# Optimization experiments

Measured on AMD Instinct MI355X. Metric: run time of the kernel, lower is better.

## Reference

```python
import jax, jax.numpy as jnp
import numpy as np

# dims: batch B, seq T, d_model C, expert_hidden H, n_experts E (top-1 routing)
B, T, C, H, E = 1, 256, 1024, 2048, 8
STD = 0.02


def setup_inputs() -> dict:
    key = jax.random.key(0)
    ks = jax.random.split(key, 8)
    f32 = jnp.float32
    return {
        "x": jax.random.normal(ks[0], (B, T, C), f32),
        "up": jax.random.normal(ks[1], (E, H, C), f32) * STD,
        "gate": jax.random.normal(ks[2], (E, H, C), f32) * STD,
        "down": jax.random.normal(ks[3], (E, C, H), f32) * STD,
        "router": jax.random.normal(ks[4], (E, C), f32) * STD,
        "w_up_s": jax.random.normal(ks[5], (H, C), f32) * STD,
        "w_gate_s": jax.random.normal(ks[6], (H, C), f32) * STD,
        "w_down_s": jax.random.normal(ks[7], (C, H), f32) * STD,
    }


def reference(x, up, gate, down, router, w_up_s, w_gate_s, w_down_s):
    b, t, c = x.shape
    x_ = x.reshape(b * t, c)                      # [BT, C]
    # top-1 router (gates are implicitly 1.0)
    logits = x_ @ router.T                        # [BT, E]
    idx = jnp.argmax(logits, axis=-1)             # [BT]
    onehot = jax.nn.one_hot(idx, router.shape[0], dtype=x.dtype)  # [BT, E]
    # dense all-expert SwiGLU, combined with one-hot (same math as per-token gather)
    u = jnp.einsum('bc,ehc->ebh', x_, up)         # [E, BT, H]
    g = jnp.einsum('bc,ehc->ebh', x_, gate)       # [E, BT, H]
    h = jax.nn.silu(g) * u                        # [E, BT, H]
    ye = jnp.einsum('ebh,ech->ebc', h, down)      # [E, BT, C]
    y = jnp.einsum('ebc,be->bc', ye, onehot)      # [BT, C]
    # shared expert residual
    ys = (jax.nn.silu(x_ @ w_gate_s.T) * (x_ @ w_up_s.T)) @ w_down_s.T
    return (y + ys).reshape(b, t, c)
```

## Files before the change

kernel.cpp:

```cpp
#include <hip/hip_runtime.h>
#include <hip/hip_bf16.h>

#define T_TOK 256
#define C_DIM 1024
#define H_DIM 2048
#define E_NUM 8

typedef __attribute__((ext_vector_type(4))) float f32x4;
typedef __attribute__((ext_vector_type(8))) short short8;

#define WS_CNT    0
#define WS_LIST   1024
#define WS_XBF    16384
#define WS_HBUF   (1u<<20)
#define WS_HSBUF  (2u<<20)
#define WS_YS     (3u<<20)

__device__ __forceinline__ ushort f2bf(float f) {
    __hip_bfloat16 h = __float2bfloat16(f);
    return *reinterpret_cast<ushort*>(&h);
}

__device__ __forceinline__ ushort4 f2bf4(float4 v) {
    ushort4 r; r.x = f2bf(v.x); r.y = f2bf(v.y); r.z = f2bf(v.z); r.w = f2bf(v.w);
    return r;
}

__device__ __forceinline__ void gload16(const void* g, void* l) {
    __builtin_amdgcn_global_load_lds((const __attribute__((address_space(1))) void*)g,
                                     (__attribute__((address_space(3))) void*)l, 16, 0, 0);
}

#define MFMA(a, b, c) __builtin_amdgcn_mfma_f32_16x16x32_bf16((a), (b), (c), 0, 0, 0)

#define VMWAIT(N) do { asm volatile("s_waitcnt vmcnt(" #N ")" ::: "memory"); \
                       __builtin_amdgcn_sched_barrier(0); } while (0)
#define LGKWAIT() do { asm volatile("s_waitcnt lgkmcnt(0)" ::: "memory"); \
                       __builtin_amdgcn_sched_barrier(0); } while (0)
#define BAR() do { __builtin_amdgcn_s_barrier(); \
                   __builtin_amdgcn_sched_barrier(0); } while (0)

__global__ __launch_bounds__(256) void router_kernel(
    const float* __restrict__ x, const float* __restrict__ router,
    int* __restrict__ cnt, int* __restrict__ list, ushort* __restrict__ xbf)
{
    const int t = blockIdx.x;
    const int tid = threadIdx.x;
    float4 xv = reinterpret_cast<const float4*>(x + (size_t)t * C_DIM)[tid];
    *reinterpret_cast<ushort4*>(xbf + (size_t)t * C_DIM + tid * 4) = f2bf4(xv);

    float p[E_NUM];
#pragma unroll
    for (int e = 0; e < E_NUM; e++) {
        float4 rv = reinterpret_cast<const float4*>(router + (size_t)e * C_DIM)[tid];
        p[e] = xv.x * rv.x + xv.y * rv.y + xv.z * rv.z + xv.w * rv.w;
    }
#pragma unroll
    for (int e = 0; e < E_NUM; e++) {
#pragma unroll
        for (int off = 32; off >= 1; off >>= 1)
            p[e] += __shfl_down(p[e], off, 64);
    }
    __shared__ float red[E_NUM][4];
    const int lane = tid & 63, wv = tid >> 6;
    if (lane == 0) {
#pragma unroll
        for (int e = 0; e < E_NUM; e++) red[e][wv] = p[e];
    }
    __syncthreads();
    if (tid == 0) {
        float best = -3.4e38f; int bi = 0;
#pragma unroll
        for (int e = 0; e < E_NUM; e++) {
            float v = red[e][0] + red[e][1] + red[e][2] + red[e][3];
            if (v > best) { best = v; bi = e; }
        }
        int pos = atomicAdd(&cnt[bi], 1);
        list[bi * T_TOK + pos] = t;
    }
}

__global__ __launch_bounds__(256, 2) void ug_mfma(
    const ushort* __restrict__ xbf, const float* __restrict__ up, const float* __restrict__ gate,
    const float* __restrict__ w_up_s, const float* __restrict__ w_gate_s,
    const int* __restrict__ cnt, const int* __restrict__ list,
    ushort* __restrict__ hbuf, ushort* __restrict__ hsbuf)
{
    const int e = blockIdx.x, by = blockIdx.y, tt = blockIdx.z;
    const bool sh = (e == E_NUM);
    const int n = sh ? T_TOK : cnt[e];
    if (tt * 32 >= n) return;
    const int tid = threadIdx.x, lane = tid & 63, wv = tid >> 6;
    const int lc = lane & 15, kg = lane >> 4;

    __shared__ __align__(16) char smem[65536];
    ushort* Xl  = (ushort*)smem;
    ushort* WuL = (ushort*)(smem + 32768);
    ushort* WgL = (ushort*)(smem + 49152);
    __shared__ int toks_s[32];

    if (tid < 32) {
        int t = tt * 32 + tid;
        toks_s[tid] = (t < n) ? (sh ? t : list[e * T_TOK + t]) : -1;
    }
    __syncthreads();

    const int h0 = by * 16;
    const float* __restrict__ ubase = (sh ? w_up_s   : up   + (size_t)e * H_DIM * C_DIM) + (size_t)h0 * C_DIM;
    const float* __restrict__ gbase = (sh ? w_gate_s : gate + (size_t)e * H_DIM * C_DIM) + (size_t)h0 * C_DIM;

    float4 wreg[8];
#define W_LOAD(tc) do { _Pragma("unroll") for (int i = 0; i < 8; i++) { \
        int row_ = wv * 4 + (i & 3); \
        const float* b_ = (i < 4) ? ubase : gbase; \
        wreg[i] = *reinterpret_cast<const float4*>(b_ + (size_t)row_ * C_DIM + (tc) * 256 + lane * 4); \
    } } while (0)

#define W_WRITE(bf) do { _Pragma("unroll") for (int i = 0; i < 8; i++) { \
        int row_ = wv * 4 + (i & 3); \
        ushort* WL_ = (i < 4) ? WuL : WgL; \
        int pos_ = ((lane >> 1) & ~7) | (((lane >> 1) ^ row_) & 7); \
        *reinterpret_cast<ushort4*>(WL_ + (bf) * 4096 + row_ * 256 + pos_ * 8 + (lane & 1) * 4) = f2bf4(wreg[i]); \
    } } while (0)

#define X_STAGE(tc, bf) do { _Pragma("unroll") for (int i = 0; i < 4; i++) { \
        int j_ = wv * 4 + i; \
        int row_ = 2 * j_ + (lane >> 5); \
        int p_ = lane & 31; \
        int su_ = (p_ & ~7) | ((p_ ^ row_) & 7); \
        int tok_ = toks_s[row_]; if (tok_ < 0) tok_ = 0; \
        gload16(xbf + (size_t)tok_ * C_DIM + (tc) * 256 + su_ * 8, (void*)(Xl + (bf) * 8192 + j_ * 512)); \
    } } while (0)

    f32x4 au0 = {0,0,0,0}, au1 = {0,0,0,0}, ag0 = {0,0,0,0}, ag1 = {0,0,0,0};
#define COMPUTE(bf) do { _Pragma("unroll") for (int k32 = 0; k32 < 2; k32++) { \
        int ku_ = wv * 8 + k32 * 4 + kg; \
        int up_ = (ku_ & ~7) | ((ku_ ^ lc) & 7); \
        short8 a0_ = *reinterpret_cast<const short8*>(Xl + (bf) * 8192 + lc * 256 + up_ * 8); \
        short8 a1_ = *reinterpret_cast<const short8*>(Xl + (bf) * 8192 + (16 + lc) * 256 + up_ * 8); \
        short8 bu_ = *reinterpret_cast<const short8*>(WuL + (bf) * 4096 + lc * 256 + up_ * 8); \
        short8 bg_ = *reinterpret_cast<const short8*>(WgL + (bf) * 4096 + lc * 256 + up_ * 8); \
        au0 = MFMA(a0_, bu_, au0); au1 = MFMA(a1_, bu_, au1); \
        ag0 = MFMA(a0_, bg_, ag0); ag1 = MFMA(a1_, bg_, ag1); \
    } } while (0)

    W_LOAD(0);
    X_STAGE(0, 0);
    VMWAIT(4);
    W_WRITE(0);
    W_LOAD(1);
    X_STAGE(1, 1);
    LGKWAIT();
    VMWAIT(12);
    BAR();

#pragma unroll
    for (int t = 0; t < 4; t++) {
        COMPUTE(t & 1);
        if (t < 3) {
            VMWAIT(4);
            W_WRITE((t + 1) & 1);
            if (t < 2) W_LOAD(t + 2);
            LGKWAIT();
        }
        BAR();
        if (t < 2) X_STAGE(t + 2, t & 1);
        if (t < 2)      { VMWAIT(12); }
        else if (t == 2){ VMWAIT(0);  }
        BAR();
    }

    f32x4* red = (f32x4*)smem;
    red[(wv * 4 + 0) * 64 + lane] = au0;
    red[(wv * 4 + 1) * 64 + lane] = au1;
    red[(wv * 4 + 2) * 64 + lane] = ag0;
    red[(wv * 4 + 3) * 64 + lane] = ag1;
    __syncthreads();
    if (tid < 128) {
        const int m = tid >> 6, ln = tid & 63, lc_ = ln & 15, kg_ = ln >> 4;
        f32x4 su = red[(0 + m) * 64 + ln];
        su += red[(4 + m) * 64 + ln];
        su += red[(8 + m) * 64 + ln];
        su += red[(12 + m) * 64 + ln];
        f32x4 sg = red[(2 + m) * 64 + ln];
        sg += red[(6 + m) * 64 + ln];
        sg += red[(10 + m) * 64 + ln];
        sg += red[(14 + m) * 64 + ln];
        ushort* __restrict__ outp = sh ? hsbuf : hbuf;
#pragma unroll
        for (int j = 0; j < 4; j++) {
            int tok = toks_s[m * 16 + kg_ * 4 + j];
            if (tok >= 0) {
                float g = sg[j], u = su[j];
                outp[(size_t)tok * H_DIM + h0 + lc_] = f2bf(u * (g / (1.f + __expf(-g))));
            }
        }
    }
#undef W_LOAD
#undef W_WRITE
#undef X_STAGE
#undef COMPUTE
}

__global__ __launch_bounds__(256, 2) void down_mfma(
    const float* __restrict__ dwn, const float* __restrict__ w_down_s,
    const ushort* __restrict__ hbuf, const ushort* __restrict__ hsbuf,
    const int* __restrict__ cnt, const int* __restrict__ list,
    float* __restrict__ y, float* __restrict__ yspart)
{
    const int e = blockIdx.x, by = blockIdx.y, tt = blockIdx.z;
    const bool sh = (e == E_NUM);
    const int n = sh ? T_TOK : cnt[e];
    if (tt * 32 >= n) return;
    const int tid = threadIdx.x, lane = tid & 63, wv = tid >> 6;
    const int lc = lane & 15, kg = lane >> 4;

    __shared__ __align__(16) char smem[49152];
    ushort* Hl  = (ushort*)smem;
    ushort* WdL = (ushort*)(smem + 32768);
    __shared__ int toks_s[32];

    if (tid < 32) {
        int t = tt * 32 + tid;
        toks_s[tid] = (t < n) ? (sh ? t : list[e * T_TOK + t]) : -1;
    }
    __syncthreads();

    const int c0 = by * 16;
    const float* __restrict__ dbase = (sh ? w_down_s : dwn + (size_t)e * C_DIM * H_DIM) + (size_t)c0 * H_DIM;
    const ushort* __restrict__ hin = sh ? hsbuf : hbuf;

    float4 wreg[4];
#define W_LOAD(tc) do { _Pragma("unroll") for (int i = 0; i < 4; i++) { \
        int row_ = wv * 4 + i; \
        wreg[i] = *reinterpret_cast<const float4*>(dbase + (size_t)row_ * H_DIM + (tc) * 256 + lane * 4); \
    } } while (0)

#define W_WRITE(bf) do { _Pragma("unroll") for (int i = 0; i < 4; i++) { \
        int row_ = wv * 4 + i; \
        int pos_ = ((lane >> 1) & ~7) | (((lane >> 1) ^ row_) & 7); \
        *reinterpret_cast<ushort4*>(WdL + (bf) * 4096 + row_ * 256 + pos_ * 8 + (lane & 1) * 4) = f2bf4(wreg[i]); \
    } } while (0)

#define H_STAGE(tc, bf) do { _Pragma("unroll") for (int i = 0; i < 4; i++) { \
        int j_ = wv * 4 + i; \
        int row_ = 2 * j_ + (lane >> 5); \
        int p_ = lane & 31; \
        int su_ = (p_ & ~7) | ((p_ ^ row_) & 7); \
        int tok_ = toks_s[row_]; if (tok_ < 0) tok_ = 0; \
        gload16(hin + (size_t)tok_ * H_DIM + (tc) * 256 + su_ * 8, (void*)(Hl + (bf) * 8192 + j_ * 512)); \
    } } while (0)

    f32x4 ac0 = {0,0,0,0}, ac1 = {0,0,0,0};
#define COMPUTE(bf) do { _Pragma("unroll") for (int k32 = 0; k32 < 2; k32++) { \
        int ku_ = wv * 8 + k32 * 4 + kg; \
        int up_ = (ku_ & ~7) | ((ku_ ^ lc) & 7); \
        short8 a0_ = *reinterpret_cast<const short8*>(Hl + (bf) * 8192 + lc * 256 + up_ * 8); \
        short8 a1_ = *reinterpret_cast<const short8*>(Hl + (bf) * 8192 + (16 + lc) * 256 + up_ * 8); \
        short8 bd_ = *reinterpret_cast<const short8*>(WdL + (bf) * 4096 + lc * 256 + up_ * 8); \
        ac0 = MFMA(a0_, bd_, ac0); ac1 = MFMA(a1_, bd_, ac1); \
    } } while (0)

    W_LOAD(0);
    H_STAGE(0, 0);
    VMWAIT(4);
    W_WRITE(0);
    W_LOAD(1);
    H_STAGE(1, 1);
    LGKWAIT();
    VMWAIT(8);
    BAR();

#pragma unroll
    for (int t = 0; t < 8; t++) {
        COMPUTE(t & 1);
        if (t < 7) {
            VMWAIT(4);
            W_WRITE((t + 1) & 1);
            if (t < 6) W_LOAD(t + 2);
            LGKWAIT();
        }
        BAR();
        if (t < 6) H_STAGE(t + 2, t & 1);
        if (t < 6)      { VMWAIT(8); }
        else if (t == 6){ VMWAIT(0); }
        BAR();
    }

    f32x4* red = (f32x4*)smem;
    red[(wv * 2 + 0) * 64 + lane] = ac0;
    red[(wv * 2 + 1) * 64 + lane] = ac1;
    __syncthreads();
    if (tid < 128) {
        const int m = tid >> 6, ln = tid & 63, lc_ = ln & 15, kg_ = ln >> 4;
        f32x4 s = red[(0 + m) * 64 + ln];
        s += red[(2 + m) * 64 + ln];
        s += red[(4 + m) * 64 + ln];
        s += red[(6 + m) * 64 + ln];
        float* __restrict__ outp = sh ? yspart : y;
#pragma unroll
        for (int j = 0; j < 4; j++) {
            int tok = toks_s[m * 16 + kg_ * 4 + j];
            if (tok >= 0) outp[(size_t)tok * C_DIM + c0 + lc_] = s[j];
        }
    }
#undef W_LOAD
#undef W_WRITE
#undef H_STAGE
#undef COMPUTE
}

__global__ __launch_bounds__(256) void add_kernel(float* __restrict__ y, const float* __restrict__ ys)
{
    int i = blockIdx.x * 256 + threadIdx.x;
    float4 a = reinterpret_cast<float4*>(y)[i];
    float4 b = reinterpret_cast<const float4*>(ys)[i];
    a.x += b.x; a.y += b.y; a.z += b.z; a.w += b.w;
    reinterpret_cast<float4*>(y)[i] = a;
}

extern "C" void kernel_launch(void* const* d_in, const int* in_sizes, int n_in,
                              void* d_out, int out_size, void* d_ws, size_t ws_size,
                              hipStream_t stream)
{
    const float* x        = (const float*)d_in[0];
    const float* up       = (const float*)d_in[1];
    const float* gate     = (const float*)d_in[2];
    const float* dwn      = (const float*)d_in[3];
    const float* router   = (const float*)d_in[4];
    const float* w_up_s   = (const float*)d_in[5];
    const float* w_gate_s = (const float*)d_in[6];
    const float* w_down_s = (const float*)d_in[7];

    char* ws = (char*)d_ws;
    int* cnt      = (int*)(ws + WS_CNT);
    int* list     = (int*)(ws + WS_LIST);
    ushort* xbf   = (ushort*)(ws + WS_XBF);
    ushort* hbuf  = (ushort*)(ws + WS_HBUF);
    ushort* hsbuf = (ushort*)(ws + WS_HSBUF);
    float* yspart = (float*)(ws + WS_YS);
    float* y = (float*)d_out;

    hipMemsetAsync(cnt, 0, E_NUM * sizeof(int), stream);
    router_kernel<<<T_TOK, 256, 0, stream>>>(x, router, cnt, list, xbf);
    ug_mfma<<<dim3(E_NUM + 1, H_DIM / 16, 8), 256, 0, stream>>>(
        xbf, up, gate, w_up_s, w_gate_s, cnt, list, hbuf, hsbuf);
    down_mfma<<<dim3(E_NUM + 1, C_DIM / 16, 8), 256, 0, stream>>>(
        dwn, w_down_s, hbuf, hsbuf, cnt, list, y, yspart);
    add_kernel<<<(T_TOK * C_DIM / 4) / 256, 256, 0, stream>>>(y, yspart);
}
```

Measured before the change: 92.57 us.

## Single-buffer ug_mfma LDS to raise occupancy and use nontemporal weight loads

Replaces the double-buffered LDS pipeline in the up/gate kernel with a single buffer, halving shared memory and raising launch bounds to three blocks per CU. The hand-scheduled waitcnt/barrier pipeline becomes a simple stage-write-sync-compute-sync loop that keeps only register prefetch of the next weight tile. Expert weights are now read with nontemporal loads to avoid cache pollution. This trades intra-block overlap of memory and MFMA for more resident waves, with added barrier stalls per iteration.

```diff
diff --git a/kernel.cpp b/kernel.cpp
--- a/kernel.cpp
+++ b/kernel.cpp
@@ -26,6 +26,11 @@
     return r;
 }
 
+__device__ __forceinline__ ushort4 f2bf4v(f32x4 v) {
+    ushort4 r; r.x = f2bf(v[0]); r.y = f2bf(v[1]); r.z = f2bf(v[2]); r.w = f2bf(v[3]);
+    return r;
+}
+
 __device__ __forceinline__ void gload16(const void* g, void* l) {
     __builtin_amdgcn_global_load_lds((const __attribute__((address_space(1))) void*)g,
                                      (__attribute__((address_space(3))) void*)l, 16, 0, 0);
@@ -80,7 +85,7 @@
     }
 }
 
-__global__ __launch_bounds__(256, 2) void ug_mfma(
+__global__ __launch_bounds__(256, 3) void ug_mfma(
     const ushort* __restrict__ xbf, const float* __restrict__ up, const float* __restrict__ gate,
     const float* __restrict__ w_up_s, const float* __restrict__ w_gate_s,
     const int* __restrict__ cnt, const int* __restrict__ list,
@@ -93,10 +98,10 @@
     const int tid = threadIdx.x, lane = tid & 63, wv = tid >> 6;
     const int lc = lane & 15, kg = lane >> 4;
 
-    __shared__ __align__(16) char smem[65536];
+    __shared__ __align__(16) char smem[32768];
     ushort* Xl  = (ushort*)smem;
-    ushort* WuL = (ushort*)(smem + 32768);
-    ushort* WgL = (ushort*)(smem + 49152);
+    ushort* WuL = (ushort*)(smem + 16384);
+    ushort* WgL = (ushort*)(smem + 24576);
     __shared__ int toks_s[32];
 
     if (tid < 32) {
@@ -109,66 +114,56 @@
     const float* __restrict__ ubase = (sh ? w_up_s   : up   + (size_t)e * H_DIM * C_DIM) + (size_t)h0 * C_DIM;
     const float* __restrict__ gbase = (sh ? w_gate_s : gate + (size_t)e * H_DIM * C_DIM) + (size_t)h0 * C_DIM;
 
-    float4 wreg[8];
+    f32x4 wreg[8];
 #define W_LOAD(tc) do { _Pragma("unroll") for (int i = 0; i < 8; i++) { \
         int row_ = wv * 4 + (i & 3); \
         const float* b_ = (i < 4) ? ubase : gbase; \
-        wreg[i] = *reinterpret_cast<const float4*>(b_ + (size_t)row_ * C_DIM + (tc) * 256 + lane * 4); \
-    } } while (0)
-
-#define W_WRITE(bf) do { _Pragma("unroll") for (int i = 0; i < 8; i++) { \
+        const f32x4* p_ = reinterpret_cast<const f32x4*>(b_ + (size_t)row_ * C_DIM + (tc) * 256 + lane * 4); \
+        wreg[i] = sh ? *p_ : __builtin_nontemporal_load(p_); \
+    } } while (0)
+
+#define W_WRITE() do { _Pragma("unroll") for (int i = 0; i < 8; i++) { \
         int row_ = wv * 4 + (i & 3); \
         ushort* WL_ = (i < 4) ? WuL : WgL; \
         int pos_ = ((lane >> 1) & ~7) | (((lane >> 1) ^ row_) & 7); \
-        *reinterpret_cast<ushort4*>(WL_ + (bf) * 4096 + row_ * 256 + pos_ * 8 + (lane & 1) * 4) = f2bf4(wreg[i]); \
-    } } while (0)
-
-#define X_STAGE(tc, bf) do { _Pragma("unroll") for (int i = 0; i < 4; i++) { \
+        *reinterpret_cast<ushort4*>(WL_ + row_ * 256 + pos_ * 8 + (lane & 1) * 4) = f2bf4v(wreg[i]); \
+    } } while (0)
+
+#define X_STAGE(tc) do { _Pragma("unroll") for (int i = 0; i < 4; i++) { \
         int j_ = wv * 4 + i; \
         int row_ = 2 * j_ + (lane >> 5); \
         int p_ = lane & 31; \
         int su_ = (p_ & ~7) | ((p_ ^ row_) & 7); \
         int tok_ = toks_s[row_]; if (tok_ < 0) tok_ = 0; \
-        gload16(xbf + (size_t)tok_ * C_DIM + (tc) * 256 + su_ * 8, (void*)(Xl + (bf) * 8192 + j_ * 512)); \
+        gload16(xbf + (size_t)tok_ * C_DIM + (tc) * 256 + su_ * 8, (void*)(Xl + j_ * 512)); \
     } } while (0)
 
     f32x4 au0 = {0,0,0,0}, au1 = {0,0,0,0}, ag0 = {0,0,0,0}, ag1 = {0,0,0,0};
-#define COMPUTE(bf) do { _Pragma("unroll") for (int k32 = 0; k32 < 2; k32++) { \
+#define COMPUTE() do { _Pragma("unroll") for (int k32 = 0; k32 < 2; k32++) { \
         int ku_ = wv * 8 + k32 * 4 + kg; \
         int up_ = (ku_ & ~7) | ((ku_ ^ lc) & 7); \
-        short8 a0_ = *reinterpret_cast<const short8*>(Xl + (bf) * 8192 + lc * 256 + up_ * 8); \
-        short8 a1_ = *reinterpret_cast<const short8*>(Xl + (bf) * 8192 + (16 + lc) * 256 + up_ * 8); \
-        short8 bu_ = *reinterpret_cast<const short8*>(WuL + (bf) * 4096 + lc * 256 + up_ * 8); \
-        short8 bg_ = *reinterpret_cast<const short8*>(WgL + (bf) * 4096 + lc * 256 + up_ * 8); \
+        short8 a0_ = *reinterpret_cast<const short8*>(Xl + lc * 256 + up_ * 8); \
+        short8 a1_ = *reinterpret_cast<const short8*>(Xl + (16 + lc) * 256 + up_ * 8); \
+        short8 bu_ = *reinterpret_cast<const short8*>(WuL + lc * 256 + up_ * 8); \
+        short8 bg_ = *reinterpret_cast<const short8*>(WgL + lc * 256 + up_ * 8); \
         au0 = MFMA(a0_, bu_, au0); au1 = MFMA(a1_, bu_, au1); \
         ag0 = MFMA(a0_, bg_, ag0); ag1 = MFMA(a1_, bg_, ag1); \
     } } while (0)
 
     W_LOAD(0);
-    X_STAGE(0, 0);
-    VMWAIT(4);
-    W_WRITE(0);
-    W_LOAD(1);
-    X_STAGE(1, 1);
-    LGKWAIT();
-    VMWAIT(12);
-    BAR();
-
 #pragma unroll
     for (int t = 0; t < 4; t++) {
-        COMPUTE(t & 1);
-        if (t < 3) {
-            VMWAIT(4);
-            W_WRITE((t + 1) & 1);
-            if (t < 2) W_LOAD(t + 2);
-            LGKWAIT();
-        }
-        BAR();
-        if (t < 2) X_STAGE(t + 2, t & 1);
-        if (t < 2)      { VMWAIT(12); }
-        else if (t == 2){ VMWAIT(0);  }
-        BAR();
-    }
+        X_STAGE(t);
+        W_WRITE();
+        if (t < 3) W_LOAD(t + 1);
+        __syncthreads();
+        COMPUTE();
+        __syncthreads();
+    }
+#undef W_LOAD
+#undef W_WRITE
+#undef X_STAGE
+#undef COMPUTE
 
     f32x4* red = (f32x4*)smem;
     red[(wv * 4 + 0) * 64 + lane] = au0;
@@ -196,10 +191,6 @@
             }
         }
     }
-#undef W_LOAD
-#undef W_WRITE
-#undef X_STAGE
-#undef COMPUTE
 }
 
 __global__ __launch_bounds__(256, 2) void down_mfma(
```

Result: faster. 90.68 us (-2.0%).
